# Optimization experiments

Hardware: AMD Instinct MI355X
Metric: run time of the kernel (lower is better)

The kernel has to match this reference:

```python
import jax, jax.numpy as jnp
import numpy as np

NUM_TAGS = 9
INNER_DIM = 64
HIDDEN = 768
MASK_VAL = 1e12


def setup_inputs() -> dict:
    key = jax.random.key(0)
    k1, k2, k3, k4 = jax.random.split(key, 4)
    B, S = 16, 512
    encoder_output = jax.random.normal(k1, (B, S, HIDDEN), dtype=jnp.float32)
    token_ids = jax.random.randint(k2, (B, S), 0, 30000, dtype=jnp.int64)
    attention_mask = jnp.ones((B, S), dtype=jnp.int32)
    W = jax.random.normal(k3, (HIDDEN, NUM_TAGS * INNER_DIM * 2), dtype=jnp.float32) * 0.02
    b = jax.random.normal(k4, (NUM_TAGS * INNER_DIM * 2,), dtype=jnp.float32) * 0.02
    return {"encoder_output": encoder_output, "token_ids": token_ids,
            "attention_mask": attention_mask, "W": W, "b": b}


def _rope_sin_cos(seq_len, dim, dtype):
    # sinusoidal position embedding, interleaved then repeat_interleave(2)
    pos = jnp.arange(seq_len, dtype=dtype)[:, None]              # [S,1]
    inv = jnp.power(10000.0, -2.0 * jnp.arange(dim // 2, dtype=dtype) / dim)
    ang = pos * inv                                              # [S,d/2]
    sin = jnp.repeat(jnp.sin(ang), 2, axis=-1)                   # [S,d]
    cos = jnp.repeat(jnp.cos(ang), 2, axis=-1)                   # [S,d]
    return sin, cos


def _rotate_half(x):
    # stack([-x[...,1::2], x[...,::2]], -1).reshape(x.shape)
    x2 = jnp.stack([-x[..., 1::2], x[..., ::2]], axis=-1)
    return x2.reshape(x.shape)


def reference(encoder_output, token_ids, attention_mask, W, b):
    B, S, _ = encoder_output.shape
    d = INNER_DIM
    out = encoder_output @ W + b                                 # [B,S,T*2d]
    out = out.reshape(B, S, NUM_TAGS, 2 * d)
    qw, kw = out[..., :d], out[..., d:]                          # [B,S,T,d]

    sin, cos = _rope_sin_cos(S, d, encoder_output.dtype)
    sin = sin[None, :, None, :]                                  # [1,S,1,d]
    cos = cos[None, :, None, :]
    qw = qw * cos + _rotate_half(qw) * sin
    kw = kw * cos + _rotate_half(kw) * sin

    logits = jnp.einsum('bshd,bthd->bhst', qw, kw)               # [B,T,S,S]

    pad = attention_mask.astype(logits.dtype)[:, None, None, :]  # key-side mask
    logits = logits * pad - (1.0 - pad) * MASK_VAL
    tril = jnp.tril(jnp.ones((S, S), dtype=logits.dtype), -1)
    logits = logits - tril * MASK_VAL
    return logits / jnp.sqrt(jnp.asarray(d, logits.dtype))
```

## Files before the change

### kernel.cpp

```cpp
#include <hip/hip_runtime.h>

#define MASK_VALF 1000000000000.0f

typedef __attribute__((ext_vector_type(8))) short s16x8;
typedef __attribute__((ext_vector_type(4))) float f32x4;

__device__ __forceinline__ unsigned f2bf_u(float f) {
    union { float f; unsigned u; } v; v.f = f;
    return (v.u + 0x7FFFu + ((v.u >> 16) & 1u)) >> 16;
}
__device__ __forceinline__ short f2bf(float f) { return (short)(f2bf_u(f) & 0xFFFFu); }

#define GLOAD16(gp, lp) __builtin_amdgcn_global_load_lds( \
    (const __attribute__((address_space(1))) void*)(gp),  \
    (__attribute__((address_space(3))) void*)(lp), 16, 0, 0)

__global__ __launch_bounds__(256) void prep_all(
    const float* __restrict__ enc, short* __restrict__ encb,
    const float* __restrict__ W, short* __restrict__ wtb,
    float* __restrict__ scf)
{
    const int blk = blockIdx.x;
    const int t = threadIdx.x;
    if (blk < 6144) {
        int i = blk * 256 + t;
        float4 v = ((const float4*)enc)[i];
        short4 o;
        o.x = f2bf(v.x); o.y = f2bf(v.y); o.z = f2bf(v.z); o.w = f2bf(v.w);
        ((short4*)encb)[i] = o;
    } else if (blk < 7008) {
        __shared__ float tile[32][33];
        int tb = blk - 6144;
        int tbx = tb % 36;
        int tby = tb / 36;
        int tx = t & 31, ty = t >> 5;
#pragma unroll
        for (int r = 0; r < 4; ++r) {
            int row = ty + r * 8;
            tile[row][tx] = W[(tby * 32 + row) * 1152 + tbx * 32 + tx];
        }
        __syncthreads();
#pragma unroll
        for (int r = 0; r < 4; ++r) {
            int row = ty + r * 8;
            wtb[(size_t)(tbx * 32 + row) * 768 + tby * 32 + tx] = f2bf(tile[tx][row]);
        }
    } else {
        int id = (blk - 7008) * 256 + t;
        int pos = id >> 5, j = id & 31;
        float inv = powf(10000.0f, -2.0f * (float)j / 64.0f);
        float ang = (float)pos * inv;
        float s, c;
        sincosf(ang, &s, &c);
        scf[id * 2]     = c;
        scf[id * 2 + 1] = s;
    }
}

__global__ __launch_bounds__(256) void gemm1_rope(
    const short* __restrict__ A,
    const short* __restrict__ Bt,
    const float* __restrict__ bias,
    const float* __restrict__ scf,
    short* __restrict__ qk)
{
    __shared__ __align__(16) short As[2][128 * 32];
    __shared__ __align__(16) short Bs[2][128 * 32];
    const int t = threadIdx.x;
    const int w = t >> 6, lane = t & 63;
    const int lr = lane & 15, quad = lane >> 4;
    const int wm = w >> 1, wn = w & 1;

    const int lin = blockIdx.y * 9 + blockIdx.x;
    const int swz = (lin & 7) * 72 + (lin >> 3);
    const int n0 = (swz % 9) * 128;
    const int m0 = (swz / 9) * 128;

    f32x4 acc[4][4] = {};

    const short* gA = A  + (size_t)(m0 + (t >> 2)) * 768 + (t & 3) * 8;
    const short* gB = Bt + (size_t)(n0 + (t >> 2)) * 768 + (t & 3) * 8;

    GLOAD16(gA,            &As[0][w * 512]);
    GLOAD16(gA + 64 * 768, &As[0][2048 + w * 512]);
    GLOAD16(gB,            &Bs[0][w * 512]);
    GLOAD16(gB + 64 * 768, &Bs[0][2048 + w * 512]);
    gA += 32; gB += 32;
    __syncthreads();

    for (int kt = 0; kt < 24; ++kt) {
        const int cur = kt & 1, nxt = cur ^ 1;
        if (kt < 23) {
            GLOAD16(gA,            &As[nxt][w * 512]);
            GLOAD16(gA + 64 * 768, &As[nxt][2048 + w * 512]);
            GLOAD16(gB,            &Bs[nxt][w * 512]);
            GLOAD16(gB + 64 * 768, &Bs[nxt][2048 + w * 512]);
            gA += 32; gB += 32;
        }
        s16x8 af[4], bw[4];
#pragma unroll
        for (int i = 0; i < 4; ++i)
            af[i] = *(const s16x8*)&Bs[cur][(wm * 64 + i * 16 + lr) * 32 + quad * 8];
#pragma unroll
        for (int j = 0; j < 4; ++j)
            bw[j] = *(const s16x8*)&As[cur][(wn * 64 + j * 16 + lr) * 32 + quad * 8];
#pragma unroll
        for (int i = 0; i < 4; ++i)
#pragma unroll
            for (int j = 0; j < 4; ++j)
                acc[i][j] = __builtin_amdgcn_mfma_f32_16x16x32_bf16(af[i], bw[j], acc[i][j], 0, 0, 0);
        __syncthreads();
    }

#pragma unroll
    for (int i = 0; i < 4; ++i) {
        const int colg0 = n0 + wm * 64 + i * 16 + quad * 4;
        const float4 bv = *(const float4*)&bias[colg0];
        const int tag = colg0 >> 7;
        const int qkf = (colg0 >> 6) & 1;
        const int dd0 = colg0 & 63;
        const int jj0 = dd0 >> 1;
        short* qbase = qk + ((size_t)tag * 2 + qkf) * 512 * 64 + dd0;
#pragma unroll
        for (int j = 0; j < 4; ++j) {
            const int rowg = m0 + wn * 64 + j * 16 + lr;
            const int bidx = rowg >> 9;
            const int pos  = rowg & 511;
            const float4 cs = *(const float4*)&scf[pos * 64 + jj0 * 2];
            float x0 = acc[i][j][0] + bv.x;
            float x1 = acc[i][j][1] + bv.y;
            float x2 = acc[i][j][2] + bv.z;
            float x3 = acc[i][j][3] + bv.w;
            float o0 = x0 * cs.x - x1 * cs.y;
            float o1 = x1 * cs.x + x0 * cs.y;
            float o2 = x2 * cs.z - x3 * cs.w;
            float o3 = x3 * cs.z + x2 * cs.w;
            int2 st;
            st.x = (int)(f2bf_u(o0) & 0xFFFFu) | (int)(f2bf_u(o1) << 16);
            st.y = (int)(f2bf_u(o2) & 0xFFFFu) | (int)(f2bf_u(o3) << 16);
            *(int2*)&qbase[((size_t)bidx * 9 * 2 * 512 + pos) * 64] = st;
        }
    }
}

__global__ __launch_bounds__(256) void gemm2_mask(
    const short* __restrict__ qk,
    const int* __restrict__ amask,
    float* __restrict__ out)
{
    const int t = threadIdx.x;
    const int w = t >> 6, lane = t & 63;
    const int lr = lane & 15, quad = lane >> 4;
    const int wm = w >> 1, wn = w & 1;
    const int bh = blockIdx.z;
    const int bidx = bh / 9;
    const int s0 = blockIdx.y * 128;
    const int t0 = blockIdx.x * 128;

    const short* qbase = qk + (size_t)bh * 2 * 512 * 64;
    const short* kbase = qbase + 512 * 64;

    const short* kf = kbase + (size_t)(t0 + wm * 64 + lr) * 64 + quad * 8;
    const short* qf = qbase + (size_t)(s0 + wn * 64 + lr) * 64 + quad * 8;

    f32x4 acc[4][4] = {};
#pragma unroll
    for (int kk = 0; kk < 64; kk += 32) {
        s16x8 af[4], bw[4];
#pragma unroll
        for (int i = 0; i < 4; ++i)
            af[i] = *(const s16x8*)&kf[i * 16 * 64 + kk];
#pragma unroll
        for (int j = 0; j < 4; ++j)
            bw[j] = *(const s16x8*)&qf[j * 16 * 64 + kk];
#pragma unroll
        for (int i = 0; i < 4; ++i)
#pragma unroll
            for (int j = 0; j < 4; ++j)
                acc[i][j] = __builtin_amdgcn_mfma_f32_16x16x32_bf16(af[i], bw[j], acc[i][j], 0, 0, 0);
    }

#pragma unroll
    for (int i = 0; i < 4; ++i) {
        const int tg0 = t0 + wm * 64 + i * 16 + quad * 4;
        const int4 am = *(const int4*)&amask[bidx * 512 + tg0];
        const float4 pad = make_float4((float)am.x, (float)am.y, (float)am.z, (float)am.w);
        const float4 mk = make_float4((1.0f - pad.x) * MASK_VALF, (1.0f - pad.y) * MASK_VALF,
                                      (1.0f - pad.z) * MASK_VALF, (1.0f - pad.w) * MASK_VALF);
#pragma unroll
        for (int j = 0; j < 4; ++j) {
            const int sg = s0 + wn * 64 + j * 16 + lr;
            f32x4 v;
            v[0] = (acc[i][j][0] * pad.x - mk.x - (sg > tg0     ? MASK_VALF : 0.0f)) * 0.125f;
            v[1] = (acc[i][j][1] * pad.y - mk.y - (sg > tg0 + 1 ? MASK_VALF : 0.0f)) * 0.125f;
            v[2] = (acc[i][j][2] * pad.z - mk.z - (sg > tg0 + 2 ? MASK_VALF : 0.0f)) * 0.125f;
            v[3] = (acc[i][j][3] * pad.w - mk.w - (sg > tg0 + 3 ? MASK_VALF : 0.0f)) * 0.125f;
            __builtin_nontemporal_store(v, (f32x4*)&out[((size_t)bh * 512 + sg) * 512 + tg0]);
        }
    }
}

extern "C" void kernel_launch(void* const* d_in, const int* in_sizes, int n_in,
                              void* d_out, int out_size, void* d_ws, size_t ws_size,
                              hipStream_t stream) {
    const float* enc   = (const float*)d_in[0];
    const int*   amask = (const int*)d_in[2];
    const float* W     = (const float*)d_in[3];
    const float* bias  = (const float*)d_in[4];
    float* out = (float*)d_out;

    char* ws = (char*)d_ws;
    short* encb = (short*)(ws);
    short* wtb  = (short*)(ws + 12582912);
    float* scf  = (float*)(ws + 14352384);
    short* qk   = (short*)(ws + 14483456);

    prep_all  <<<7072, 256, 0, stream>>>(enc, encb, W, wtb, scf);
    gemm1_rope<<<dim3(9, 64), 256, 0, stream>>>(encb, wtb, bias, scf, qk);
    gemm2_mask<<<dim3(4, 4, 144), 256, 0, stream>>>(qk, amask, out);
}
```

Before: 234.7 us.

## Fuse fp32-to-bf16 encoder conversion into GEMM1 tile loads; use plain output stores

The separate pass that converted the encoder output to bf16 is removed. GEMM1 now loads fp32 encoder tiles straight into LDS and converts them to bf16 while building the MFMA fragments, which saves a full write and re-read of a 12 MB intermediate. The cost is twice the LDS footprint for the A tiles, double the A global-load traffic per K step, and conversion ALU work repeated across the 9 column blocks. Separately, GEMM2 switches from nontemporal stores to ordinary vector stores.

```diff
diff --git a/kernel.cpp b/kernel.cpp
--- a/kernel.cpp
+++ b/kernel.cpp
@@ -16,23 +16,15 @@
     (__attribute__((address_space(3))) void*)(lp), 16, 0, 0)
 
 __global__ __launch_bounds__(256) void prep_all(
-    const float* __restrict__ enc, short* __restrict__ encb,
     const float* __restrict__ W, short* __restrict__ wtb,
     float* __restrict__ scf)
 {
     const int blk = blockIdx.x;
     const int t = threadIdx.x;
-    if (blk < 6144) {
-        int i = blk * 256 + t;
-        float4 v = ((const float4*)enc)[i];
-        short4 o;
-        o.x = f2bf(v.x); o.y = f2bf(v.y); o.z = f2bf(v.z); o.w = f2bf(v.w);
-        ((short4*)encb)[i] = o;
-    } else if (blk < 7008) {
+    if (blk < 864) {
         __shared__ float tile[32][33];
-        int tb = blk - 6144;
-        int tbx = tb % 36;
-        int tby = tb / 36;
+        int tbx = blk % 36;
+        int tby = blk / 36;
         int tx = t & 31, ty = t >> 5;
 #pragma unroll
         for (int r = 0; r < 4; ++r) {
@@ -46,7 +38,7 @@
             wtb[(size_t)(tbx * 32 + row) * 768 + tby * 32 + tx] = f2bf(tile[tx][row]);
         }
     } else {
-        int id = (blk - 7008) * 256 + t;
+        int id = (blk - 864) * 256 + t;
         int pos = id >> 5, j = id & 31;
         float inv = powf(10000.0f, -2.0f * (float)j / 64.0f);
         float ang = (float)pos * inv;
@@ -58,13 +50,13 @@
 }
 
 __global__ __launch_bounds__(256) void gemm1_rope(
-    const short* __restrict__ A,
+    const float* __restrict__ enc,
     const short* __restrict__ Bt,
     const float* __restrict__ bias,
     const float* __restrict__ scf,
     short* __restrict__ qk)
 {
-    __shared__ __align__(16) short As[2][128 * 32];
+    __shared__ __align__(16) float As[2][128 * 32];
     __shared__ __align__(16) short Bs[2][128 * 32];
     const int t = threadIdx.x;
     const int w = t >> 6, lane = t & 63;
@@ -78,11 +70,12 @@
 
     f32x4 acc[4][4] = {};
 
-    const short* gA = A  + (size_t)(m0 + (t >> 2)) * 768 + (t & 3) * 8;
+    const float* gA = enc + (size_t)(m0 + w * 32 + (lane >> 3)) * 768 + (lane & 7) * 4;
     const short* gB = Bt + (size_t)(n0 + (t >> 2)) * 768 + (t & 3) * 8;
 
-    GLOAD16(gA,            &As[0][w * 512]);
-    GLOAD16(gA + 64 * 768, &As[0][2048 + w * 512]);
+#pragma unroll
+    for (int p = 0; p < 4; ++p)
+        GLOAD16(gA + (size_t)p * 8 * 768, &As[0][(w * 32 + p * 8) * 32]);
     GLOAD16(gB,            &Bs[0][w * 512]);
     GLOAD16(gB + 64 * 768, &Bs[0][2048 + w * 512]);
     gA += 32; gB += 32;
@@ -91,8 +84,9 @@
     for (int kt = 0; kt < 24; ++kt) {
         const int cur = kt & 1, nxt = cur ^ 1;
         if (kt < 23) {
-            GLOAD16(gA,            &As[nxt][w * 512]);
-            GLOAD16(gA + 64 * 768, &As[nxt][2048 + w * 512]);
+#pragma unroll
+            for (int p = 0; p < 4; ++p)
+                GLOAD16(gA + (size_t)p * 8 * 768, &As[nxt][(w * 32 + p * 8) * 32]);
             GLOAD16(gB,            &Bs[nxt][w * 512]);
             GLOAD16(gB + 64 * 768, &Bs[nxt][2048 + w * 512]);
             gA += 32; gB += 32;
@@ -102,8 +96,15 @@
         for (int i = 0; i < 4; ++i)
             af[i] = *(const s16x8*)&Bs[cur][(wm * 64 + i * 16 + lr) * 32 + quad * 8];
 #pragma unroll
-        for (int j = 0; j < 4; ++j)
-            bw[j] = *(const s16x8*)&As[cur][(wn * 64 + j * 16 + lr) * 32 + quad * 8];
+        for (int j = 0; j < 4; ++j) {
+            const float* fr = &As[cur][(wn * 64 + j * 16 + lr) * 32 + quad * 8];
+            const f32x4 lo = *(const f32x4*)&fr[0];
+            const f32x4 hi = *(const f32x4*)&fr[4];
+            s16x8 b;
+            b[0] = f2bf(lo[0]); b[1] = f2bf(lo[1]); b[2] = f2bf(lo[2]); b[3] = f2bf(lo[3]);
+            b[4] = f2bf(hi[0]); b[5] = f2bf(hi[1]); b[6] = f2bf(hi[2]); b[7] = f2bf(hi[3]);
+            bw[j] = b;
+        }
 #pragma unroll
         for (int i = 0; i < 4; ++i)
 #pragma unroll
@@ -190,12 +191,12 @@
 #pragma unroll
         for (int j = 0; j < 4; ++j) {
             const int sg = s0 + wn * 64 + j * 16 + lr;
-            f32x4 v;
-            v[0] = (acc[i][j][0] * pad.x - mk.x - (sg > tg0     ? MASK_VALF : 0.0f)) * 0.125f;
-            v[1] = (acc[i][j][1] * pad.y - mk.y - (sg > tg0 + 1 ? MASK_VALF : 0.0f)) * 0.125f;
-            v[2] = (acc[i][j][2] * pad.z - mk.z - (sg > tg0 + 2 ? MASK_VALF : 0.0f)) * 0.125f;
-            v[3] = (acc[i][j][3] * pad.w - mk.w - (sg > tg0 + 3 ? MASK_VALF : 0.0f)) * 0.125f;
-            __builtin_nontemporal_store(v, (f32x4*)&out[((size_t)bh * 512 + sg) * 512 + tg0]);
+            float4 v;
+            v.x = (acc[i][j][0] * pad.x - mk.x - (sg > tg0     ? MASK_VALF : 0.0f)) * 0.125f;
+            v.y = (acc[i][j][1] * pad.y - mk.y - (sg > tg0 + 1 ? MASK_VALF : 0.0f)) * 0.125f;
+            v.z = (acc[i][j][2] * pad.z - mk.z - (sg > tg0 + 2 ? MASK_VALF : 0.0f)) * 0.125f;
+            v.w = (acc[i][j][3] * pad.w - mk.w - (sg > tg0 + 3 ? MASK_VALF : 0.0f)) * 0.125f;
+            *(float4*)&out[((size_t)bh * 512 + sg) * 512 + tg0] = v;
         }
     }
 }
@@ -210,12 +211,11 @@
     float* out = (float*)d_out;
 
     char* ws = (char*)d_ws;
-    short* encb = (short*)(ws);
-    short* wtb  = (short*)(ws + 12582912);
-    float* scf  = (float*)(ws + 14352384);
-    short* qk   = (short*)(ws + 14483456);
-
-    prep_all  <<<7072, 256, 0, stream>>>(enc, encb, W, wtb, scf);
-    gemm1_rope<<<dim3(9, 64), 256, 0, stream>>>(encb, wtb, bias, scf, qk);
+    short* wtb  = (short*)(ws);
+    float* scf  = (float*)(ws + 1769472);
+    short* qk   = (short*)(ws + 1900544);
+
+    prep_all  <<<928, 256, 0, stream>>>(W, wtb, scf);
+    gemm1_rope<<<dim3(9, 64), 256, 0, stream>>>(enc, wtb, bias, scf, qk);
     gemm2_mask<<<dim3(4, 4, 144), 256, 0, stream>>>(qk, amask, out);
 }
```

Result: slower. 263.3 us (+12.2%).
